# Optimization experiments

Measured on AMD Instinct MI355X. Metric: run time of the kernel, lower is better.

Reference implementation:

```python
import jax, jax.numpy as jnp
import numpy as np
from jax import lax

# dims
B, T = 64, 1024
ANNOT, RNN, MEM, ATTN = 512, 1024, 512, 512
FILTERS, KSIZE = 32, 31
PAD = (KSIZE - 1) // 2  # 15, SAME padding


def setup_inputs() -> dict:
    key = jax.random.key(0)
    ks = jax.random.split(key, 20)
    s = 0.02
    return {
        "memory": jax.random.normal(ks[0], (B, MEM), jnp.float32),
        "context": jax.random.normal(ks[1], (B, ANNOT), jnp.float32),
        "rnn_state": jax.random.normal(ks[2], (B, RNN), jnp.float32),
        "annots": jax.random.normal(ks[3], (B, T, ANNOT), jnp.float32),
        "atten": jax.random.uniform(ks[4], (B, 2, T), jnp.float32),
        "mask": jnp.ones((B, T), jnp.int32),
        "t": 0,
        # GRUCell params (torch gate order: r, z, n)
        "W_ih": jax.random.normal(ks[5], (3 * RNN, ANNOT + MEM), jnp.float32) * s,
        "W_hh": jax.random.normal(ks[6], (3 * RNN, RNN), jnp.float32) * s,
        "b_ih": jnp.zeros((3 * RNN,), jnp.float32),
        "b_hh": jnp.zeros((3 * RNN,), jnp.float32),
        # location-sensitive attention params
        "conv_w": jax.random.normal(ks[7], (FILTERS, 2, KSIZE), jnp.float32) * s,
        "loc_w": jax.random.normal(ks[8], (ATTN, FILTERS), jnp.float32) * s,
        "loc_b": jnp.zeros((ATTN,), jnp.float32),
        "q_w": jax.random.normal(ks[9], (ATTN, RNN), jnp.float32) * s,
        "q_b": jnp.zeros((ATTN,), jnp.float32),
        "a_w": jax.random.normal(ks[10], (ATTN, ANNOT), jnp.float32) * s,
        "a_b": jnp.zeros((ATTN,), jnp.float32),
        "v_w": jax.random.normal(ks[11], (1, ATTN), jnp.float32) * s,
    }


def _gru_cell(x, h, W_ih, W_hh, b_ih, b_hh):
    gi = x @ W_ih.T + b_ih  # [B, 3H]
    gh = h @ W_hh.T + b_hh
    i_r, i_z, i_n = jnp.split(gi, 3, axis=-1)
    h_r, h_z, h_n = jnp.split(gh, 3, axis=-1)
    r = jax.nn.sigmoid(i_r + h_r)
    z = jax.nn.sigmoid(i_z + h_z)
    n = jnp.tanh(i_n + r * h_n)
    return (1.0 - z) * n + z * h


def reference(memory, context, rnn_state, annots, atten, mask, t,
              W_ih, W_hh, b_ih, b_hh, conv_w, loc_w, loc_b,
              q_w, q_b, a_w, a_b, v_w):
    # GRU step on [memory; prev_context]
    rnn_input = jnp.concatenate([memory, context], axis=-1)  # [B, MEM+ANNOT]
    rnn_output = _gru_cell(rnn_input, rnn_state, W_ih, W_hh, b_ih, b_hh)  # [B, RNN]

    # location features: SAME conv over [B, 2, T] -> [B, FILTERS, T]
    loc_conv = lax.conv_general_dilated(
        atten, conv_w, window_strides=(1,), padding=[(PAD, PAD)],
        dimension_numbers=("NCH", "OIH", "NCH"))
    processed_loc = jnp.einsum("bft,af->bta", loc_conv, loc_w) + loc_b  # [B,T,ATTN]

    processed_query = (rnn_output @ q_w.T + q_b)[:, None, :]            # [B,1,ATTN]
    processed_annots = jnp.einsum("btd,ad->bta", annots, a_w) + a_b     # [B,T,ATTN]

    energy = jnp.tanh(processed_query + processed_annots + processed_loc)
    alignment = jnp.einsum("bta,a->bt", energy, v_w[0])                 # [B,T]

    # mask fill with -inf where mask == 0
    alignment = jnp.where(mask == 0, -jnp.inf, alignment)

    # sigmoid-normalized attention weights
    sig = jax.nn.sigmoid(alignment)
    alignment = sig / jnp.sum(sig, axis=1, keepdims=True)               # [B,T]

    new_context = jnp.einsum("bt,btd->bd", alignment, annots)           # [B,ANNOT]
    return rnn_output, new_context, alignment
```

## Files before the change

### kernel.cpp

```cpp
#include <hip/hip_runtime.h>

typedef float f32x4 __attribute__((ext_vector_type(4)));
typedef short bf16x8 __attribute__((ext_vector_type(8)));

__device__ __forceinline__ unsigned int pk2(float a, float b) {
    unsigned int ua = __float_as_uint(a); ua += 0x7FFFu + ((ua >> 16) & 1u);
    unsigned int ub = __float_as_uint(b); ub += 0x7FFFu + ((ub >> 16) & 1u);
    return __builtin_amdgcn_perm(ub, ua, 0x07060302u);
}
__device__ __forceinline__ unsigned short bf16_rne(float a) {
    unsigned int ua = __float_as_uint(a);
    ua += 0x7FFFu + ((ua >> 16) & 1u);
    return (unsigned short)(ua >> 16);
}
__device__ __forceinline__ float tanh_fast(float x) {
    float e = __expf(x + x);
    return 1.f - 2.f / (e + 1.f);
}
__device__ __forceinline__ f32x4 mfma16(bf16x8 a, bf16x8 b, f32x4 c) {
    return __builtin_amdgcn_mfma_f32_16x16x32_bf16(a, b, c, 0, 0, 0);
}
__device__ __forceinline__ void ald16(const void* g, void* l) {
    __builtin_amdgcn_global_load_lds(
        (const __attribute__((address_space(1))) unsigned int*)g,
        (__attribute__((address_space(3))) unsigned int*)l, 16, 0, 0);
}

#define Q_WIH   786432
#define Q_WHH   1572864
#define Q_QW    1703936
#define Q_X2    1720320
#define Q_X1    1736704
#define Q_BAW   1802240
#define Q_BLW   1806336
#define Q_EB    1806464
#define NCVT    7057

__global__ __launch_bounds__(256) void k_prep(
    const float* __restrict__ Wih, const float* __restrict__ Whh,
    const float* __restrict__ qw, const float* __restrict__ rnn_state,
    const float* __restrict__ memory, const float* __restrict__ context,
    const float* __restrict__ aw, const float* __restrict__ lw,
    const float* __restrict__ ab, const float* __restrict__ lb,
    const float* __restrict__ atten, const float* __restrict__ convw,
    unsigned short* __restrict__ Wihb, unsigned short* __restrict__ Whhb,
    unsigned short* __restrict__ qwb, unsigned short* __restrict__ X2b,
    unsigned short* __restrict__ X1b, unsigned short* __restrict__ Bbig,
    float* __restrict__ ebias, unsigned short* __restrict__ Lconv)
{
    __shared__ float att_s[2 * 160];
    __shared__ float cw_s[1984];
    const int tid = threadIdx.x;
    if (blockIdx.x < NCVT) {
        int q = blockIdx.x * 256 + tid;
        if (q >= Q_EB) return;
        if (q < Q_WIH) {
            int i = q * 4;
            float4 v = *(const float4*)(Wih + i);
            uint2 u; u.x = pk2(v.x, v.y); u.y = pk2(v.z, v.w);
            *(uint2*)(Wihb + i) = u;
        } else if (q < Q_WHH) {
            int i = (q - Q_WIH) * 4;
            float4 v = *(const float4*)(Whh + i);
            uint2 u; u.x = pk2(v.x, v.y); u.y = pk2(v.z, v.w);
            *(uint2*)(Whhb + i) = u;
        } else if (q < Q_QW) {
            int i = (q - Q_WHH) * 4;
            float4 v = *(const float4*)(qw + i);
            uint2 u; u.x = pk2(v.x, v.y); u.y = pk2(v.z, v.w);
            *(uint2*)(qwb + i) = u;
        } else if (q < Q_X2) {
            int i = (q - Q_QW) * 4;
            float4 v = *(const float4*)(rnn_state + i);
            uint2 u; u.x = pk2(v.x, v.y); u.y = pk2(v.z, v.w);
            *(uint2*)(X2b + i) = u;
        } else if (q < Q_X1) {
            int i = (q - Q_X2) * 4;
            int b = i >> 10, c = i & 1023;
            const float* s = (c < 512) ? (memory + b * 512 + c) : (context + b * 512 + (c - 512));
            float4 v = *(const float4*)s;
            uint2 u; u.x = pk2(v.x, v.y); u.y = pk2(v.z, v.w);
            *(uint2*)(X1b + i) = u;
        } else if (q < Q_BAW) {
            int i = (q - Q_X1) * 4;
            int a = i >> 9, c = i & 511;
            float4 v = *(const float4*)(aw + a * 512 + c);
            uint2 u; u.x = pk2(v.x, v.y); u.y = pk2(v.z, v.w);
            *(uint2*)(Bbig + a * 544 + c) = u;
        } else if (q < Q_BLW) {
            int i = (q - Q_BAW) * 4;
            int a = i >> 5, c = i & 31;
            float4 v = *(const float4*)(lw + a * 32 + c);
            uint2 u; u.x = pk2(v.x, v.y); u.y = pk2(v.z, v.w);
            *(uint2*)(Bbig + a * 544 + 512 + c) = u;
        } else {
            int i = (q - Q_BLW) * 4;
            float4 va = *(const float4*)(ab + i);
            float4 vb = *(const float4*)(lb + i);
            float4 r; r.x = va.x + vb.x; r.y = va.y + vb.y; r.z = va.z + vb.z; r.w = va.w + vb.w;
            *(float4*)(ebias + i) = r;
        }
    } else {
        const int bid = blockIdx.x - NCVT;
        const int b = bid >> 3;
        const int tbase = (bid & 7) * 128;
        for (int i = tid; i < 320; i += 256) {
            int c = i / 160, j = i % 160;
            float v = 0.f;
            int pos = tbase - 15 + j;
            if (j < 158 && pos >= 0 && pos < 1024) v = atten[b * 2048 + c * 1024 + pos];
            att_s[c * 160 + j] = v;
        }
        for (int i = tid; i < 1984; i += 256) cw_s[i] = convw[i];
        __syncthreads();
        const int f = tid & 31, tq = tid >> 5;
        float acc[16];
#pragma unroll
        for (int i = 0; i < 16; ++i) acc[i] = 0.f;
        for (int c = 0; c < 2; ++c) {
            for (int k = 0; k < 31; ++k) {
                float w = cw_s[f * 62 + c * 31 + k];
                int base = c * 160 + tq * 16 + k;
#pragma unroll
                for (int ti = 0; ti < 16; ++ti) acc[ti] += w * att_s[base + ti];
            }
        }
#pragma unroll
        for (int ti = 0; ti < 16; ++ti) {
            int t = tbase + tq * 16 + ti;
            Lconv[(b * 1024 + t) * 32 + f] = bf16_rne(acc[ti]);
        }
    }
}

__global__ __launch_bounds__(256, 4) void k_gemm_ks(
    const unsigned short* __restrict__ A1, const unsigned short* __restrict__ A2,
    const unsigned short* __restrict__ B1, const unsigned short* __restrict__ B2,
    float* __restrict__ C, int N, int nTiles, int n_split, int K, int Klen)
{
    __shared__ __align__(16) unsigned short As[64 * 32];
    __shared__ __align__(16) unsigned short Bs[128 * 32];
    const int tid = threadIdx.x;
    const int nb = blockIdx.x % nTiles;
    const int ks = blockIdx.x / nTiles;
    const int nBase = nb * 128;
    const bool use2 = nBase >= n_split;
    const unsigned short* A = use2 ? A2 : A1;
    const unsigned short* B = use2 ? B2 : B1;
    const int brow0 = nBase - (use2 ? n_split : 0);
    const int lane = tid & 63, w = tid >> 6;
    const int c = lane & 15, qd = lane >> 4;
    const int lr = lane >> 2;
    const int swzl = ((lane & 3) ^ ((lr >> 1) & 3)) * 8;

    const f32x4 fz = {0.f, 0.f, 0.f, 0.f};
    f32x4 acc[4][2];
#pragma unroll
    for (int i = 0; i < 4; ++i) { acc[i][0] = fz; acc[i][1] = fz; }

    const int k0b = ks * Klen;
    const int nkc = Klen >> 5;
    for (int kc = 0; kc < nkc; ++kc) {
        const int k0 = k0b + kc * 32;
        ald16(A + (size_t)(w * 16 + lr) * K + k0 + swzl, &As[w * 512]);
        ald16(B + (size_t)(brow0 + w * 16 + lr) * K + k0 + swzl, &Bs[w * 512]);
        ald16(B + (size_t)(brow0 + 64 + w * 16 + lr) * K + k0 + swzl, &Bs[2048 + w * 512]);
        __syncthreads();
        const int rdoff = (qd ^ ((c >> 1) & 3)) * 8;
        bf16x8 af[4];
#pragma unroll
        for (int i = 0; i < 4; ++i) af[i] = *(const bf16x8*)&As[(i * 16 + c) * 32 + rdoff];
#pragma unroll
        for (int j = 0; j < 2; ++j) {
            bf16x8 bj = *(const bf16x8*)&Bs[(w * 32 + j * 16 + c) * 32 + rdoff];
#pragma unroll
            for (int i = 0; i < 4; ++i) acc[i][j] = mfma16(af[i], bj, acc[i][j]);
        }
        __syncthreads();
    }
    float* Cp = C + (size_t)ks * 64 * N;
#pragma unroll
    for (int i = 0; i < 4; ++i)
#pragma unroll
        for (int r = 0; r < 4; ++r) {
            int row = i * 16 + qd * 4 + r;
#pragma unroll
            for (int j = 0; j < 2; ++j) {
                int col = nBase + w * 32 + j * 16 + c;
                Cp[row * N + col] = acc[i][j][r];
            }
        }
}

__global__ __launch_bounds__(256) void k_gates(
    const float* __restrict__ Cg, const float* __restrict__ h0,
    const float* __restrict__ bih, const float* __restrict__ bhh,
    float* __restrict__ outv, unsigned short* __restrict__ X3b)
{
    int idx = blockIdx.x * 256 + threadIdx.x;
    int b = idx >> 10, h = idx & 1023;
    const float* g0 = Cg + b * 6144;
    const float* g1 = Cg + 393216 + b * 6144;
    float ir = g0[h] + g1[h] + bih[h];
    float iz = g0[h + 1024] + g1[h + 1024] + bih[h + 1024];
    float inn = g0[h + 2048] + g1[h + 2048] + bih[h + 2048];
    float hr = g0[h + 3072] + g1[h + 3072] + bhh[h];
    float hz = g0[h + 4096] + g1[h + 4096] + bhh[h + 1024];
    float hn = g0[h + 5120] + g1[h + 5120] + bhh[h + 2048];
    float r = 1.f / (1.f + __expf(-(ir + hr)));
    float z = 1.f / (1.f + __expf(-(iz + hz)));
    float n = tanh_fast(inn + r * hn);
    float o = (1.f - z) * n + z * h0[idx];
    outv[idx] = o;
    X3b[idx] = bf16_rne(o);
}

__global__ __launch_bounds__(256, 2) void k_attn(
    const float* __restrict__ annots, const unsigned short* __restrict__ Lconv,
    const unsigned short* __restrict__ Bbig, const float* __restrict__ pqP,
    const float* __restrict__ qb, const float* __restrict__ ebias,
    const float* __restrict__ vw, float* __restrict__ wsal)
{
    __shared__ __align__(16) unsigned short As[64 * 32];
    __shared__ __align__(16) unsigned short Bs[512 * 32];
    __shared__ float red[4][64];
    const int tid = threadIdx.x;
    const int btBase = blockIdx.x * 64;
    const int b = btBase >> 10;
    const int lane = tid & 63, w = tid >> 6;
    const int c = lane & 15, qd = lane >> 4;
    const int lr = lane >> 2;
    const int swzl = ((lane & 3) ^ ((lr >> 1) & 3)) * 8;
    const int arow = tid >> 2, alc = tid & 3;
    const int apofs = (alc ^ ((arow >> 1) & 3)) * 8;

    const f32x4 fz = {0.f, 0.f, 0.f, 0.f};
    f32x4 acc[4][8];
#pragma unroll
    for (int i = 0; i < 4; ++i)
#pragma unroll
        for (int j = 0; j < 8; ++j) acc[i][j] = fz;

    for (int kc = 0; kc < 17; ++kc) {
        const int k0 = kc * 32;
#pragma unroll
        for (int s = 0; s < 8; ++s)
            ald16(Bbig + (size_t)(s * 64 + w * 16 + lr) * 544 + k0 + swzl,
                  &Bs[s * 2048 + w * 512]);
        if (kc < 16) {
            const float* p = annots + (size_t)(btBase + arow) * 512 + k0 + alc * 8;
            float4 v0 = *(const float4*)p;
            float4 v1 = *(const float4*)(p + 4);
            uint4 u;
            u.x = pk2(v0.x, v0.y); u.y = pk2(v0.z, v0.w);
            u.z = pk2(v1.x, v1.y); u.w = pk2(v1.z, v1.w);
            *(uint4*)&As[arow * 32 + apofs] = u;
        } else {
            ald16(Lconv + (size_t)(btBase + w * 16 + lr) * 32 + swzl, &As[w * 512]);
        }
        __syncthreads();
        const int rdoff = (qd ^ ((c >> 1) & 3)) * 8;
        bf16x8 af[4];
#pragma unroll
        for (int i = 0; i < 4; ++i) af[i] = *(const bf16x8*)&As[(i * 16 + c) * 32 + rdoff];
#pragma unroll
        for (int j = 0; j < 8; ++j) {
            bf16x8 bj = *(const bf16x8*)&Bs[(w * 128 + j * 16 + c) * 32 + rdoff];
#pragma unroll
            for (int i = 0; i < 4; ++i) acc[i][j] = mfma16(af[i], bj, acc[i][j]);
        }
        __syncthreads();
    }
    float pe[8], vv[8];
#pragma unroll
    for (int j = 0; j < 8; ++j) {
        int colg = w * 128 + j * 16 + c;
        pe[j] = pqP[b * 512 + colg] + pqP[32768 + b * 512 + colg] + qb[colg] + ebias[colg];
        vv[j] = vw[colg];
    }
#pragma unroll
    for (int i = 0; i < 4; ++i)
#pragma unroll
        for (int r = 0; r < 4; ++r) {
            float p = 0.f;
#pragma unroll
            for (int j = 0; j < 8; ++j)
                p += vv[j] * tanh_fast(acc[i][j][r] + pe[j]);
            p += __shfl_xor(p, 1);
            p += __shfl_xor(p, 2);
            p += __shfl_xor(p, 4);
            p += __shfl_xor(p, 8);
            if (c == 0) red[w][i * 16 + qd * 4 + r] = p;
        }
    __syncthreads();
    if (tid < 64)
        wsal[btBase + tid] = red[0][tid] + red[1][tid] + red[2][tid] + red[3][tid];
}

__global__ __launch_bounds__(256) void k_ctx(
    const float* __restrict__ annots, const float* __restrict__ wsal,
    const int* __restrict__ mask, float* __restrict__ out)
{
    __shared__ float al[1024];
    __shared__ float wsum[4];
    __shared__ float red[256];
    const int b = blockIdx.x >> 3;
    const int chunk = blockIdx.x & 7;
    const int tid = threadIdx.x;
    float lsum = 0.f;
#pragma unroll
    for (int p = 0; p < 4; ++p) {
        int t = p * 256 + tid;
        int bt = b * 1024 + t;
        float raw = wsal[bt];
        float s = (mask[bt] != 0) ? 1.f / (1.f + __expf(-raw)) : 0.f;
        al[t] = s;
        lsum += s;
    }
    for (int off = 32; off > 0; off >>= 1) lsum += __shfl_xor(lsum, off);
    if ((tid & 63) == 0) wsum[tid >> 6] = lsum;
    __syncthreads();
    const float tot = wsum[0] + wsum[1] + wsum[2] + wsum[3];
    const float inv = 1.f / tot;
    if (chunk == 0) {
#pragma unroll
        for (int p = 0; p < 4; ++p) {
            int t = p * 256 + tid;
            out[98304 + b * 1024 + t] = al[t] * inv;
        }
    }
    const int dq = tid & 63, tq = tid >> 6;
    const int d = chunk * 64 + dq;
    const float* ap = annots + (size_t)(b * 1024 + tq * 256) * 512 + d;
    float acc = 0.f;
#pragma unroll 4
    for (int t = 0; t < 256; ++t) acc += al[tq * 256 + t] * ap[(size_t)t * 512];
    red[tid] = acc;
    __syncthreads();
    if (tid < 64) {
        float s2 = red[tid] + red[64 + tid] + red[128 + tid] + red[192 + tid];
        out[65536 + b * 512 + chunk * 64 + tid] = s2 * inv;
    }
}

extern "C" void kernel_launch(void* const* d_in, const int* in_sizes, int n_in,
                              void* d_out, int out_size, void* d_ws, size_t ws_size,
                              hipStream_t stream) {
    const float* memory    = (const float*)d_in[0];
    const float* context   = (const float*)d_in[1];
    const float* rnn_state = (const float*)d_in[2];
    const float* annots    = (const float*)d_in[3];
    const float* atten     = (const float*)d_in[4];
    const int*   mask      = (const int*)d_in[5];
    const float* W_ih   = (const float*)d_in[7];
    const float* W_hh   = (const float*)d_in[8];
    const float* b_ih   = (const float*)d_in[9];
    const float* b_hh   = (const float*)d_in[10];
    const float* conv_w = (const float*)d_in[11];
    const float* loc_w  = (const float*)d_in[12];
    const float* loc_b  = (const float*)d_in[13];
    const float* q_w    = (const float*)d_in[14];
    const float* q_b    = (const float*)d_in[15];
    const float* a_w    = (const float*)d_in[16];
    const float* a_b    = (const float*)d_in[17];
    const float* v_w    = (const float*)d_in[18];
    float* out = (float*)d_out;

    char* w8 = (char*)d_ws;
    unsigned short* Lconv = (unsigned short*)(w8 + 0);
    unsigned short* Bbig  = (unsigned short*)(w8 + 4194304);
    unsigned short* Wihb  = (unsigned short*)(w8 + 4751360);
    unsigned short* Whhb  = (unsigned short*)(w8 + 11042816);
    unsigned short* qwb   = (unsigned short*)(w8 + 17334272);
    unsigned short* X1b   = (unsigned short*)(w8 + 18382848);
    unsigned short* X2b   = (unsigned short*)(w8 + 18513920);
    unsigned short* X3b   = (unsigned short*)(w8 + 18644992);
    float*          Cgru  = (float*)(w8 + 18776064);
    float*          pqP   = (float*)(w8 + 18776064);
    float*          wsal  = (float*)(w8 + 19038208);
    float*          ebias = (float*)(w8 + 21921792);

    k_prep<<<NCVT + 512, 256, 0, stream>>>(W_ih, W_hh, q_w, rnn_state, memory, context,
                                           a_w, loc_w, a_b, loc_b, atten, conv_w,
                                           Wihb, Whhb, qwb, X2b, X1b, Bbig, ebias, Lconv);
    k_gemm_ks<<<96, 256, 0, stream>>>(X1b, X2b, Wihb, Whhb, Cgru, 6144, 48, 3072, 1024, 512);
    k_gates<<<256, 256, 0, stream>>>(Cgru, rnn_state, b_ih, b_hh, out, X3b);
    k_gemm_ks<<<8, 256, 0, stream>>>(X3b, X3b, qwb, qwb, pqP, 512, 4, 0x40000000, 1024, 512);
    k_attn<<<1024, 256, 0, stream>>>(annots, Lconv, Bbig, pqP, q_b, ebias, v_w, wsal);
    k_ctx<<<512, 256, 0, stream>>>(annots, wsal, mask, out);
}
```

Before: 349.1 us.

## Double-buffer LDS tiles in attention GEMM to overlap loads with MFMA

```diff
diff --git a/kernel.cpp b/kernel.cpp
--- a/kernel.cpp
+++ b/kernel.cpp
@@ -221,8 +221,8 @@
     const float* __restrict__ qb, const float* __restrict__ ebias,
     const float* __restrict__ vw, float* __restrict__ wsal)
 {
-    __shared__ __align__(16) unsigned short As[64 * 32];
-    __shared__ __align__(16) unsigned short Bs[512 * 32];
+    __shared__ __align__(16) unsigned short As[2][64 * 32];
+    __shared__ __align__(16) unsigned short Bs[2][512 * 32];
     __shared__ float red[4][64];
     const int tid = threadIdx.x;
     const int btBase = blockIdx.x * 64;
@@ -241,35 +241,58 @@
 #pragma unroll
         for (int j = 0; j < 8; ++j) acc[i][j] = fz;
 
+    const float* aP = annots + (size_t)(btBase + arow) * 512 + alc * 8;
+    const unsigned short* bP = Bbig + (size_t)(w * 16 + lr) * 544 + swzl;
+
+#pragma unroll
+    for (int s = 0; s < 8; ++s)
+        ald16(bP + (size_t)s * 64 * 544, &Bs[0][s * 2048 + w * 512]);
+    {
+        float4 v0 = *(const float4*)(aP);
+        float4 v1 = *(const float4*)(aP + 4);
+        uint4 u;
+        u.x = pk2(v0.x, v0.y); u.y = pk2(v0.z, v0.w);
+        u.z = pk2(v1.x, v1.y); u.w = pk2(v1.z, v1.w);
+        *(uint4*)&As[0][arow * 32 + apofs] = u;
+    }
+    __syncthreads();
+
     for (int kc = 0; kc < 17; ++kc) {
-        const int k0 = kc * 32;
-#pragma unroll
-        for (int s = 0; s < 8; ++s)
-            ald16(Bbig + (size_t)(s * 64 + w * 16 + lr) * 544 + k0 + swzl,
-                  &Bs[s * 2048 + w * 512]);
+        const int cur = kc & 1, nxt = cur ^ 1;
+        float4 v0n, v1n;
         if (kc < 16) {
-            const float* p = annots + (size_t)(btBase + arow) * 512 + k0 + alc * 8;
-            float4 v0 = *(const float4*)p;
-            float4 v1 = *(const float4*)(p + 4);
-            uint4 u;
-            u.x = pk2(v0.x, v0.y); u.y = pk2(v0.z, v0.w);
-            u.z = pk2(v1.x, v1.y); u.w = pk2(v1.z, v1.w);
-            *(uint4*)&As[arow * 32 + apofs] = u;
-        } else {
-            ald16(Lconv + (size_t)(btBase + w * 16 + lr) * 32 + swzl, &As[w * 512]);
-        }
-        __syncthreads();
+            const int k1 = (kc + 1) * 32;
+#pragma unroll
+            for (int s = 0; s < 8; ++s)
+                ald16(bP + (size_t)s * 64 * 544 + k1, &Bs[nxt][s * 2048 + w * 512]);
+            if (kc < 15) {
+                v0n = *(const float4*)(aP + k1);
+                v1n = *(const float4*)(aP + k1 + 4);
+            } else {
+                ald16(Lconv + (size_t)(btBase + w * 16 + lr) * 32 + swzl, &As[nxt][w * 512]);
+            }
+        }
         const int rdoff = (qd ^ ((c >> 1) & 3)) * 8;
         bf16x8 af[4];
 #pragma unroll
-        for (int i = 0; i < 4; ++i) af[i] = *(const bf16x8*)&As[(i * 16 + c) * 32 + rdoff];
+        for (int i = 0; i < 4; ++i) af[i] = *(const bf16x8*)&As[cur][(i * 16 + c) * 32 + rdoff];
+        __builtin_amdgcn_s_setprio(1);
 #pragma unroll
         for (int j = 0; j < 8; ++j) {
-            bf16x8 bj = *(const bf16x8*)&Bs[(w * 128 + j * 16 + c) * 32 + rdoff];
+            bf16x8 bj = *(const bf16x8*)&Bs[cur][(w * 128 + j * 16 + c) * 32 + rdoff];
 #pragma unroll
             for (int i = 0; i < 4; ++i) acc[i][j] = mfma16(af[i], bj, acc[i][j]);
         }
-        __syncthreads();
+        __builtin_amdgcn_s_setprio(0);
+        if (kc < 16) {
+            if (kc < 15) {
+                uint4 u;
+                u.x = pk2(v0n.x, v0n.y); u.y = pk2(v0n.z, v0n.w);
+                u.z = pk2(v1n.x, v1n.y); u.w = pk2(v1n.z, v1n.w);
+                *(uint4*)&As[nxt][arow * 32 + apofs] = u;
+            }
+            __syncthreads();
+        }
     }
     float pe[8], vv[8];
 #pragma unroll
```

Result: no change. 342.9 us (-1.8%).
